# Kernel tuning notes

Hardware: AMD Instinct MI355X
Metric: run time of the kernel (lower is better)

Reference implementation:

```python
import jax, jax.numpy as jnp
import numpy as np
import math

N_FUNC = 32
LR_START, LR_DECAY = 1.0, 0.977
WEIGHT_DECAY, AMP_DECAY, MM_LR = 0.01, 0.01, 0.03
N_SAMP, BATCH, MOMENTUM = 32, 16, 0.85
N_FEAT, N_TARGET, MEM_SIZE = 1024, 512, 16384
DATA_SIZE = 100
SQRT_NF = math.sqrt(N_FUNC)


def setup_inputs() -> dict:
    key = jax.random.key(0)
    ks = jax.random.split(key, 16)
    p = jnp.linspace(0.01, 0.99, N_FUNC)[:, None]
    center_freq = jnp.log(p / (1.0 - p))  # logit of linspace, as in __init__
    return {
        "t": DATA_SIZE,
        "data_size": DATA_SIZE,
        "ts": jax.random.randint(ks[0], (N_SAMP,), 0, DATA_SIZE + 1),
        "x": jax.random.normal(ks[1], (N_FEAT,), jnp.float32),
        "z": jax.random.normal(ks[2], (N_TARGET,), jnp.float32),
        "memory": jax.random.normal(ks[3], (MEM_SIZE, N_TARGET), jnp.float32),
        "t_memory": jax.random.randint(ks[4], (MEM_SIZE,), 0, DATA_SIZE),
        "feat_memory": jax.random.normal(ks[5], (MEM_SIZE, N_FEAT), jnp.float32),
        "amp_re": 1.0 / SQRT_NF + 0.01 * jax.random.normal(ks[6], (N_FUNC, N_TARGET), jnp.float32),
        "amp_im": 0.01 * jax.random.normal(ks[7], (N_FUNC, N_TARGET), jnp.float32),
        "freq": 0.1 * jax.random.normal(ks[8], (N_FUNC, 1), jnp.float32),
        "center_freq": center_freq.astype(jnp.float32),
        "res_proj": 0.02 * jax.random.normal(ks[9], (N_FEAT + N_TARGET, N_TARGET), jnp.float32),
        "feat_mean": 0.1 * jax.random.normal(ks[10], (N_FEAT,), jnp.float32),
        "bias": 0.1 * jax.random.normal(ks[11], (N_TARGET,), jnp.float32),
        "amp_grad_re": 0.01 * jax.random.normal(ks[12], (N_FUNC, N_TARGET), jnp.float32),
        "amp_grad_im": 0.01 * jax.random.normal(ks[13], (N_FUNC, N_TARGET), jnp.float32),
        "freq_grad": 0.01 * jax.random.normal(ks[14], (N_FUNC, 1), jnp.float32),
        "res_proj_grad": 0.001 * jax.random.normal(ks[15], (N_FEAT + N_TARGET, N_TARGET), jnp.float32),
    }


def _get_freq(freq, center_freq):
    fr = center_freq + jnp.tanh(freq) * (64.0 / N_FUNC)
    return jax.nn.sigmoid(fr) * 0.5


def _evaluate(t, amp_re, amp_im, freq, bias, center_freq):
    # t: [B]; amp: [F, T]; freq/center_freq: [F, 1]
    fr = _get_freq(freq, center_freq)                      # [F, 1]
    ph = (2.0 * math.pi) * t[:, None, None] * fr           # [B, F, 1]
    # Re(exp(i*ph) * (amp_re + i*amp_im)) = cos*amp_re - sin*amp_im
    z = (jnp.cos(ph) * amp_re - jnp.sin(ph) * amp_im).sum(1) / SQRT_NF
    return z + bias                                        # [B, T]


def _get_resid(x, z, res_proj, feat_mean, bias):
    r = jnp.concatenate([x - feat_mean, z - bias], axis=-1) @ res_proj
    return r / (jnp.abs(r) + 1.0)


def reference(t, data_size, ts, x, z, memory, t_memory, feat_memory,
              amp_re, amp_im, freq, center_freq, res_proj, feat_mean, bias,
              amp_grad_re, amp_grad_im, freq_grad, res_proj_grad):
    # scatter new sample into the ring buffers
    memory = memory.at[data_size].set(z)
    feat_memory = feat_memory.at[data_size].set(x)
    t_memory = t_memory.at[data_size].set(t)
    ds_new = data_size + 1
    lr = LR_START * LR_DECAY ** ds_new  # lr after this call's decay
    # running means (torch uses the already-incremented data_size)
    bias = (bias * ds_new + z) / (ds_new + 1)
    feat_mean = (feat_mean * ds_new + x) / (ds_new + 1)

    for b in range(N_SAMP // BATCH):
        batch = ts[b * BATCH:(b + 1) * BATCH]
        t_b = t_memory[batch].astype(jnp.float32)
        z_b = memory[batch]
        x_b = feat_memory[batch]

        def loss_fn(a_re, a_im, fq, rp):
            z_ = _evaluate(t_b, a_re, a_im, fq, bias, center_freq)
            amp_abs = jnp.sqrt(a_re ** 2 + a_im ** 2)
            loss = jnp.sqrt(amp_abs).sum() * AMP_DECAY
            loss = loss + jnp.abs(z_b - z_).sum(-1).mean()
            resid = _get_resid(x_b, z_, rp, feat_mean, bias)
            z2 = jax.lax.stop_gradient(z_) + resid
            res_loss = jnp.abs(z_b - z2).sum(-1).mean()
            # torch uses self.res_proj (buffer) here -> no grad through this term
            res_loss = res_loss + jnp.abs(jax.lax.stop_gradient(rp)).sum() * WEIGHT_DECAY
            return loss + res_loss * MM_LR

        ag_re, ag_im, fg, rg = jax.grad(loss_fn, argnums=(0, 1, 2, 3))(amp_re, amp_im, freq, res_proj)
        # momentum decay then normalized-grad accumulate, then SGD step
        anorm = jnp.sqrt((ag_re ** 2).sum() + (ag_im ** 2).sum()) + 1.0  # complex vector norm
        amp_grad_re = amp_grad_re * MOMENTUM + ag_re / anorm
        amp_grad_im = amp_grad_im * MOMENTUM + ag_im / anorm
        amp_re = amp_re - amp_grad_re * lr
        amp_im = amp_im - amp_grad_im * lr
        fnorm = jnp.sqrt((fg ** 2).sum()) + 1.0
        freq_grad = freq_grad * MOMENTUM + fg / fnorm
        freq = freq - freq_grad * lr
        rnorm = jnp.sqrt((rg ** 2).sum()) + 1.0
        res_proj_grad = res_proj_grad * MOMENTUM + rg / rnorm
        res_proj = res_proj - res_proj_grad * lr

    return (memory, t_memory, feat_memory, amp_re, amp_im, freq, res_proj,
            bias, feat_mean, amp_grad_re, amp_grad_im, freq_grad, res_proj_grad)
```

## Files before the change

kernel.cpp:

```cpp
#include <hip/hip_runtime.h>
#include <math.h>

#define NT 512
#define NF 1024
#define NFUNC 32
#define BATCHSZ 16

typedef float v4f __attribute__((ext_vector_type(4)));
typedef int   v4i __attribute__((ext_vector_type(4)));

constexpr int O_MEM  = 0;
constexpr int O_TMEM = 8388608;
constexpr int O_FEAT = 8404992;
constexpr int O_ARE  = 25182208;
constexpr int O_AIM  = 25198592;
constexpr int O_FREQ = 25214976;
constexpr int O_RP   = 25215008;
constexpr int O_BIAS = 26001440;
constexpr int O_FM   = 26001952;
constexpr int O_AGR  = 26002976;
constexpr int O_AGI  = 26019360;
constexpr int O_FGR  = 26035744;
constexpr int O_RPG  = 26035776;

constexpr int W_LR    = 0;
constexpr int W_ANORM = 2;
constexpr int W_RNORM = 4;
constexpr int W_GFR   = 8;
constexpr int W_TB    = 72;
constexpr int W_C     = 96;
constexpr int W_S     = 608;
constexpr int W_CATZ  = 1120;
constexpr int W_CATX  = 9312;
constexpr int W_GR    = 25696;
constexpr int W_G     = 33888;
constexpr int W_AGRE  = 42080;
constexpr int W_AGIM  = 58464;
constexpr int W_RPART = 74848;

constexpr float MM_LR = 0.03f;
constexpr float AMP_DECAY = 0.01f;
constexpr float MOM = 0.85f;
constexpr float INV_SQRT_NF = 0.17677669529663687f;
constexpr float TWO_PI = 6.283185307179586f;

constexpr int NCOPY = 256;
constexpr long long U_TOTAL = 6295552LL;

constexpr int R_MEM_END  = 2097152;
constexpr int R_FEAT_END = 6291456;
constexpr int R_TM_END   = 6295552;

__device__ __forceinline__ float sgnf(float x) {
    return (x > 0.f) ? 1.f : ((x < 0.f) ? -1.f : 0.f);
}

__device__ __forceinline__ float wave_reduce(float v) {
#pragma unroll
    for (int o = 32; o > 0; o >>= 1) v += __shfl_down(v, o, 64);
    return v;
}

__device__ __forceinline__ void copy_role(int rb, int cbase, int ccnt,
    const int* __restrict__ tptr, const int* __restrict__ dsptr,
    const float* __restrict__ x, const float* __restrict__ z,
    const float* __restrict__ memory, const int* __restrict__ t_memory,
    const float* __restrict__ feat_memory, float* __restrict__ out)
{
    const int dsv  = *dsptr;
    const int nthr = NCOPY * 256;
    const int tg   = rb * 256 + (int)threadIdx.x;
    const int cend = cbase + ccnt;

    {
        const int a1 = cend < R_MEM_END ? cend : R_MEM_END;
        const v4f* __restrict__ src = (const v4f*)memory;
        const v4f* __restrict__ zz  = (const v4f*)z;
        v4f* __restrict__ dst = (v4f*)(out + O_MEM);
        int u = cbase + tg;
        for (; u + 3 * nthr < a1; u += 4 * nthr) {
            const int u1 = u + nthr, u2 = u + 2 * nthr, u3 = u + 3 * nthr;
            v4f v0 = __builtin_nontemporal_load((u  >> 7) == dsv ? zz + (u  & 127) : src + u );
            v4f v1 = __builtin_nontemporal_load((u1 >> 7) == dsv ? zz + (u1 & 127) : src + u1);
            v4f v2 = __builtin_nontemporal_load((u2 >> 7) == dsv ? zz + (u2 & 127) : src + u2);
            v4f v3 = __builtin_nontemporal_load((u3 >> 7) == dsv ? zz + (u3 & 127) : src + u3);
            __builtin_nontemporal_store(v0, dst + u );
            __builtin_nontemporal_store(v1, dst + u1);
            __builtin_nontemporal_store(v2, dst + u2);
            __builtin_nontemporal_store(v3, dst + u3);
        }
        for (; u < a1; u += nthr) {
            v4f v = __builtin_nontemporal_load((u >> 7) == dsv ? zz + (u & 127) : src + u);
            __builtin_nontemporal_store(v, dst + u);
        }
    }
    {
        const int a0 = cbase > R_MEM_END ? cbase : R_MEM_END;
        const int a1 = cend < R_FEAT_END ? cend : R_FEAT_END;
        const v4f* __restrict__ src = (const v4f*)feat_memory;
        const v4f* __restrict__ xx  = (const v4f*)x;
        v4f* __restrict__ dst = (v4f*)(out + O_FEAT);
        int u = a0 + tg;
        for (; u + 3 * nthr < a1; u += 4 * nthr) {
            const int u1 = u + nthr, u2 = u + 2 * nthr, u3 = u + 3 * nthr;
            const int f0 = u - R_MEM_END, f1 = u1 - R_MEM_END,
                      f2 = u2 - R_MEM_END, f3 = u3 - R_MEM_END;
            v4f v0 = __builtin_nontemporal_load((f0 >> 8) == dsv ? xx + (f0 & 255) : src + f0);
            v4f v1 = __builtin_nontemporal_load((f1 >> 8) == dsv ? xx + (f1 & 255) : src + f1);
            v4f v2 = __builtin_nontemporal_load((f2 >> 8) == dsv ? xx + (f2 & 255) : src + f2);
            v4f v3 = __builtin_nontemporal_load((f3 >> 8) == dsv ? xx + (f3 & 255) : src + f3);
            __builtin_nontemporal_store(v0, dst + f0);
            __builtin_nontemporal_store(v1, dst + f1);
            __builtin_nontemporal_store(v2, dst + f2);
            __builtin_nontemporal_store(v3, dst + f3);
        }
        for (; u < a1; u += nthr) {
            const int f = u - R_MEM_END;
            v4f v = __builtin_nontemporal_load((f >> 8) == dsv ? xx + (f & 255) : src + f);
            __builtin_nontemporal_store(v, dst + f);
        }
    }
    {
        const int a0 = cbase > R_FEAT_END ? cbase : R_FEAT_END;
        const int a1 = cend;
        if (a1 > a0) {
            const float ft = (float)(*tptr);
            const v4i* __restrict__ tm = (const v4i*)t_memory;
            v4f* __restrict__ dst = (v4f*)(out + O_TMEM);
            for (int u = a0 + tg; u < a1; u += nthr) {
                const int f = u - R_FEAT_END;
                const v4i iv = __builtin_nontemporal_load(tm + f);
                const int e = f * 4;
                v4f v;
                v.x = (e + 0 == dsv) ? ft : (float)iv.x;
                v.y = (e + 1 == dsv) ? ft : (float)iv.y;
                v.z = (e + 2 == dsv) ? ft : (float)iv.z;
                v.w = (e + 3 == dsv) ? ft : (float)iv.w;
                __builtin_nontemporal_store(v, dst + f);
            }
        }
    }
}

#define COPY_ARGS const int* __restrict__ tptr, const int* __restrict__ dsptr,            \
                  const float* __restrict__ x, const float* __restrict__ z,               \
                  const float* __restrict__ memory, const int* __restrict__ t_memory,     \
                  const float* __restrict__ feat_memory, int cbase, int ccnt
#define COPY_PASS tptr, dsptr, x, z, memory, t_memory, feat_memory

__global__ __launch_bounds__(256) void k_fwd_ab(int b, const int* __restrict__ ts,
    const float* __restrict__ cf,
    const float* __restrict__ are_src, const float* __restrict__ aim_src,
    const float* __restrict__ fq_src, const float* __restrict__ fm_in,
    const float* __restrict__ rp_src,
    float* __restrict__ out, float* __restrict__ ws, COPY_ARGS)
{
    int bb = blockIdx.x;
    const int tid = threadIdx.x;
    if (bb < NCOPY) { copy_role(bb, cbase, ccnt, COPY_PASS, out); return; }
    bb -= NCOPY;
    const int i = bb >> 4, s = bb & 15;
    __shared__ float c_l[32], s_l[32], cat[96];
    const int dsv = *dsptr;
    const int bi = ts[b * BATCHSZ + i];
    if (tid < 32) {
        float f  = fq_src[tid];
        float th = tanhf(f);
        float u  = cf[tid] + 2.f * th;
        float sg = 1.f / (1.f + expf(-u));
        float fr = 0.5f * sg;
        float tb = (bi == dsv) ? (float)(*tptr) : (float)t_memory[bi];
        float ph = TWO_PI * tb * fr;
        float cv = cosf(ph), sv = sinf(ph);
        c_l[tid] = cv; s_l[tid] = sv;
        if (s == 0) {
            ws[W_C + i*32 + tid] = cv; ws[W_S + i*32 + tid] = sv;
            if (tid == 0) ws[W_TB + i] = tb;
        }
    }
    if (bb == 0) {
        if (tid == 64) ws[W_ANORM + b] = 0.f;
        if (tid == 65) ws[W_RNORM + b] = 0.f;
        if (tid == 66 && b == 0) ws[W_LR] = (float)pow(0.977, (double)(dsv + 1));
        if (tid >= 96 && tid < 128) ws[W_GFR + b*32 + tid - 96] = 0.f;
    }
    __syncthreads();
    if (tid < 96) {
        int p = s * 96 + tid;
        float cv;
        if (p < NF) {
            const float nn = (float)(dsv + 1), dd = (float)(dsv + 2);
            float fmv = (fm_in[p] * nn + x[p]) / dd;
            float xv  = (bi == dsv) ? x[p] : feat_memory[bi*NF + p];
            cv = xv - fmv;
            ws[W_CATX + i*NF + p] = cv;
        } else {
            int q = p - NF;
            float acc = 0.f;
#pragma unroll
            for (int k = 0; k < 32; ++k)
                acc += c_l[k] * are_src[k*NT + q] - s_l[k] * aim_src[k*NT + q];
            cv = acc * INV_SQRT_NF;
            ws[W_CATZ + i*NT + q] = cv;
        }
        cat[tid] = cv;
    }
    __syncthreads();
    const int j = tid;
    const float* rpb = rp_src + (size_t)s * 96 * NT;
    float a0 = 0.f, a1 = 0.f, b0 = 0.f, b1 = 0.f;
#pragma unroll 8
    for (int p = 0; p < 96; p += 2) {
        float c0 = cat[p], c1 = cat[p + 1];
        a0 += c0 * rpb[p*NT + j];
        a1 += c0 * rpb[p*NT + j + 256];
        b0 += c1 * rpb[(p+1)*NT + j];
        b1 += c1 * rpb[(p+1)*NT + j + 256];
    }
    ws[W_RPART + s*8192 + i*NT + j]       = a0 + b0;
    ws[W_RPART + s*8192 + i*NT + j + 256] = a1 + b1;
}

__global__ __launch_bounds__(256) void k_eplg3(int b, const int* __restrict__ ts,
    const float* __restrict__ bias_in, const float* __restrict__ fm_in,
    const float* __restrict__ rp_src,
    float* __restrict__ out, float* __restrict__ ws, COPY_ARGS)
{
    int bb = blockIdx.x;
    const int tid = threadIdx.x;
    if (bb < NCOPY) { copy_role(bb, cbase, ccnt, COPY_PASS, out); return; }
    bb -= NCOPY;
    const int i = bb >> 6, jg = bb & 63;
    __shared__ float g_sh[NT], d_sh[NT];
    const int dsv = *dsptr;
    const int bi = ts[b * BATCHSZ + i];
    const float nn = (float)(dsv + 1), dd = (float)(dsv + 2);
#pragma unroll
    for (int ll = 0; ll < 2; ++ll) {
        int l = tid + ll * 256;
        float r = 0.f;
#pragma unroll
        for (int s = 0; s < 16; ++s) r += ws[W_RPART + s*8192 + i*NT + l];
        float bn = (bias_in[l] * nn + z[l]) / dd;
        float zj = ws[W_CATZ + i*NT + l] + bn;
        float zb = (bi == dsv) ? z[l] : memory[bi*NT + l];
        float s1 = sgnf(zj - zb);
        float ar = fabsf(r) + 1.f;
        float z2 = zj + r / ar;
        float g  = sgnf(z2 - zb) * (MM_LR / 16.f) / (ar * ar);
        g_sh[l] = g; d_sh[l] = s1 * (1.f / 16.f);
        if (jg == 0) {
            ws[W_GR + i*NT + l] = g;
            if (b == 0 && i == 0) out[O_BIAS + l] = bn;
        }
    }
    if (b == 0 && jg == 0 && i < 2) {
#pragma unroll
        for (int ll = 0; ll < 2; ++ll) {
            int p = i * 512 + tid + ll * 256;
            out[O_FM + p] = (fm_in[p] * nn + x[p]) / dd;
        }
    }
    __syncthreads();
    const int w = tid >> 6, lane = tid & 63;
#pragma unroll
    for (int jj = 0; jj < 2; ++jj) {
        int j = jg * 8 + w * 2 + jj;
        const float* rrow = rp_src + (size_t)(NF + j) * NT;
        float acc = 0.f;
#pragma unroll
        for (int l = lane; l < NT; l += 64) acc += g_sh[l] * rrow[l];
        acc = wave_reduce(acc);
        if (lane == 0) ws[W_G + i*NT + j] = d_sh[j] + acc;
    }
}

__global__ __launch_bounds__(256) void k_norms(int b,
    const float* __restrict__ are_src, const float* __restrict__ aim_src,
    float* __restrict__ out, float* __restrict__ ws, COPY_ARGS)
{
    __shared__ float red[4];
    int bb = blockIdx.x;
    const int tid = threadIdx.x;
    if (bb < NCOPY) { copy_role(bb, cbase, ccnt, COPY_PASS, out); return; }
    bb -= NCOPY;
    if (bb < 64) {
        int e = bb*256 + tid;
        int k = e >> 9;
        float gre = 0.f, gim = 0.f;
#pragma unroll
        for (int i2 = 0; i2 < 16; ++i2) {
            float G = ws[W_G + i2*NT + (e & 511)];
            gre += G * ws[W_C + i2*32 + k];
            gim += G * ws[W_S + i2*32 + k];
        }
        float re = are_src[e], im = aim_src[e];
        float aa = sqrtf(re*re + im*im);
        float dec = AMP_DECAY / (2.f * aa * sqrtf(aa));
        float agr =  gre * INV_SQRT_NF + re * dec;
        float agi = -gim * INV_SQRT_NF + im * dec;
        ws[W_AGRE + e] = agr;
        ws[W_AGIM + e] = agi;
        float v = wave_reduce(agr*agr + agi*agi);
        if ((tid & 63) == 0) red[tid >> 6] = v;
        __syncthreads();
        if (tid == 0) atomicAdd(&ws[W_ANORM + b], red[0]+red[1]+red[2]+red[3]);
    } else if (bb < 192) {
        int wid = tid >> 6, lane = tid & 63;
        int pair = (bb - 64)*4 + wid;
        int i = pair >> 5, k = pair & 31;
        float ck = ws[W_C + i*32 + k], sk = ws[W_S + i*32 + k];
        float acc = 0.f;
#pragma unroll
        for (int j = lane; j < NT; j += 64)
            acc += ws[W_G + i*NT + j] * (-sk * are_src[k*NT + j] - ck * aim_src[k*NT + j]);
        acc = wave_reduce(acc);
        if (lane == 0)
            atomicAdd(&ws[W_GFR + b*32 + k], acc * TWO_PI * ws[W_TB + i] * INV_SQRT_NF);
    } else {
        int e = (bb - 192)*256 + tid;
        int p = e >> 9, j = e & 511;
        float rg = 0.f;
#pragma unroll
        for (int i2 = 0; i2 < 16; ++i2) {
            float cat = (p < NF) ? ws[W_CATX + i2*NF + p]
                                 : ws[W_CATZ + i2*NT + (p - NF)];
            rg += cat * ws[W_GR + i2*NT + j];
        }
        float v = wave_reduce(rg * rg);
        if ((tid & 63) == 0) red[tid >> 6] = v;
        __syncthreads();
        if (tid == 0) atomicAdd(&ws[W_RNORM + b], red[0]+red[1]+red[2]+red[3]);
    }
}

__global__ __launch_bounds__(256) void k_upd(int b, const float* __restrict__ cf,
    const float* __restrict__ are_src, const float* __restrict__ aim_src,
    const float* __restrict__ agr_src, const float* __restrict__ agi_src,
    const float* __restrict__ fq_src,  const float* __restrict__ fgr_src,
    const float* __restrict__ rp_src,  const float* __restrict__ rpg_src,
    float* __restrict__ out, float* __restrict__ ws, COPY_ARGS)
{
    int bb = blockIdx.x;
    const int tid = threadIdx.x;
    if (bb < NCOPY) { copy_role(bb, cbase, ccnt, COPY_PASS, out); return; }
    bb -= NCOPY;
    const float lr = ws[W_LR];
    if (bb < 64) {
        int e = bb*256 + tid;
        float anorm = sqrtf(ws[W_ANORM + b]) + 1.f;
        float mr = agr_src[e]*MOM + ws[W_AGRE + e]/anorm;
        out[O_AGR + e] = mr; out[O_ARE + e] = are_src[e] - mr*lr;
        float mi = agi_src[e]*MOM + ws[W_AGIM + e]/anorm;
        out[O_AGI + e] = mi; out[O_AIM + e] = aim_src[e] - mi*lr;
    } else if (bb == 64) {
        if (tid < 64) {
            float fg = 0.f, th = 0.f;
            if (tid < 32) {
                float f = fq_src[tid];
                th = tanhf(f);
                float u  = cf[tid] + 2.f*th;
                float sg = 1.f / (1.f + expf(-u));
                fg = ws[W_GFR + b*32 + tid] * sg*(1.f-sg)*(1.f-th*th);
            }
            float t2 = fg*fg;
#pragma unroll
            for (int o = 32; o > 0; o >>= 1) t2 += __shfl_down(t2, o, 64);
            float tot = __shfl(t2, 0, 64);
            if (tid < 32) {
                float fnorm = sqrtf(tot) + 1.f;
                float m = fgr_src[tid]*MOM + fg/fnorm;
                out[O_FGR + tid] = m;
                out[O_FREQ + tid] = fq_src[tid] - m*lr;
            }
        }
    } else {
        int e = (bb - 65)*256 + tid;
        int p = e >> 9, j = e & 511;
        float rg = 0.f;
#pragma unroll
        for (int i2 = 0; i2 < 16; ++i2) {
            float cat = (p < NF) ? ws[W_CATX + i2*NF + p]
                                 : ws[W_CATZ + i2*NT + (p - NF)];
            rg += cat * ws[W_GR + i2*NT + j];
        }
        float rnorm = sqrtf(ws[W_RNORM + b]) + 1.f;
        float m = rpg_src[e]*MOM + rg/rnorm;
        out[O_RPG + e] = m; out[O_RP + e] = rp_src[e] - m*lr;
    }
}

extern "C" void kernel_launch(void* const* d_in, const int* in_sizes, int n_in,
                              void* d_out, int out_size, void* d_ws, size_t ws_size,
                              hipStream_t stream)
{
    const int*   t            = (const int*)d_in[0];
    const int*   dsp          = (const int*)d_in[1];
    const int*   ts           = (const int*)d_in[2];
    const float* x            = (const float*)d_in[3];
    const float* z            = (const float*)d_in[4];
    const float* memory       = (const float*)d_in[5];
    const int*   t_memory     = (const int*)d_in[6];
    const float* feat_memory  = (const float*)d_in[7];
    const float* amp_re       = (const float*)d_in[8];
    const float* amp_im       = (const float*)d_in[9];
    const float* freq         = (const float*)d_in[10];
    const float* cf           = (const float*)d_in[11];
    const float* res_proj     = (const float*)d_in[12];
    const float* feat_mean    = (const float*)d_in[13];
    const float* bias         = (const float*)d_in[14];
    const float* amp_grad_re  = (const float*)d_in[15];
    const float* amp_grad_im  = (const float*)d_in[16];
    const float* freq_grad    = (const float*)d_in[17];
    const float* res_proj_grad= (const float*)d_in[18];
    float* out = (float*)d_out;
    float* ws  = (float*)d_ws;

    const float* ARE[2] = { amp_re,        out + O_ARE };
    const float* AIM[2] = { amp_im,        out + O_AIM };
    const float* AGR[2] = { amp_grad_re,   out + O_AGR };
    const float* AGI[2] = { amp_grad_im,   out + O_AGI };
    const float* FQ [2] = { freq,          out + O_FREQ };
    const float* FGR[2] = { freq_grad,     out + O_FGR };
    const float* RP [2] = { res_proj,      out + O_RP };
    const float* RPG[2] = { res_proj_grad, out + O_RPG };

    const int per = 786944;
    int base = 0;
    auto nxt = [&](int& cb, int& cc) { cb = base; cc = per; base += cc; };
    int cb, cc;
    for (int b = 0; b < 2; ++b) {
        nxt(cb, cc);
        k_fwd_ab<<<256 + NCOPY, 256, 0, stream>>>(b, ts, cf, ARE[b], AIM[b], FQ[b],
            feat_mean, RP[b], out, ws, t, dsp, x, z, memory, t_memory, feat_memory, cb, cc);
        nxt(cb, cc);
        k_eplg3<<<1024 + NCOPY, 256, 0, stream>>>(b, ts, bias, feat_mean, RP[b], out, ws,
            t, dsp, x, z, memory, t_memory, feat_memory, cb, cc);
        nxt(cb, cc);
        k_norms<<<3264 + NCOPY, 256, 0, stream>>>(b, ARE[b], AIM[b], out, ws,
            t, dsp, x, z, memory, t_memory, feat_memory, cb, cc);
        nxt(cb, cc);
        k_upd<<<3137 + NCOPY, 256, 0, stream>>>(b, cf, ARE[b], AIM[b], AGR[b], AGI[b],
            FQ[b], FGR[b], RP[b], RPG[b], out, ws,
            t, dsp, x, z, memory, t_memory, feat_memory, cb, cc);
    }
}
```

Before: 333.1 us.

## Fuse multi-kernel training step into one cooperative persistent kernel with grid syncs

Replaces the sequence of per-stage kernel launches (two iterations, several stages each) with a single cooperative kernel of 512 blocks. Grid-wide syncs act as the stage boundaries, and the bulk memory copy is split into chunks placed between stages to overlap with compute. The aim is to remove launch overhead and inter-kernel gaps. In exchange it adds grid-barrier costs, halves the copy-loop unroll, and depends on cooperative launch support, falling back to the old path if that is missing.

```diff
diff --git a/kernel.cpp b/kernel.cpp
--- a/kernel.cpp
+++ b/kernel.cpp
@@ -1,5 +1,8 @@
 #include <hip/hip_runtime.h>
+#include <hip/hip_cooperative_groups.h>
 #include <math.h>
+
+namespace cg = cooperative_groups;
 
 #define NT 512
 #define NF 1024
@@ -44,12 +47,22 @@
 constexpr float INV_SQRT_NF = 0.17677669529663687f;
 constexpr float TWO_PI = 6.283185307179586f;
 
+constexpr int NB = 512;
+constexpr int CHUNK = 786944;
 constexpr int NCOPY = 256;
-constexpr long long U_TOTAL = 6295552LL;
 
 constexpr int R_MEM_END  = 2097152;
 constexpr int R_FEAT_END = 6291456;
-constexpr int R_TM_END   = 6295552;
+
+struct KParams {
+    const int *t, *dsp, *ts;
+    const float *x, *z, *memory;
+    const int *t_memory;
+    const float *feat_memory;
+    const float *amp_re, *amp_im, *freq, *cf, *res_proj, *feat_mean, *bias;
+    const float *amp_grad_re, *amp_grad_im, *freq_grad, *res_proj_grad;
+    float *out, *ws;
+};
 
 __device__ __forceinline__ float sgnf(float x) {
     return (x > 0.f) ? 1.f : ((x < 0.f) ? -1.f : 0.f);
@@ -61,33 +74,24 @@
     return v;
 }
 
-__device__ __forceinline__ void copy_role(int rb, int cbase, int ccnt,
-    const int* __restrict__ tptr, const int* __restrict__ dsptr,
+__device__ __forceinline__ void copy_span(int tg, int nthr, int cbase, int cend,
+    int dsv, int tt,
     const float* __restrict__ x, const float* __restrict__ z,
     const float* __restrict__ memory, const int* __restrict__ t_memory,
     const float* __restrict__ feat_memory, float* __restrict__ out)
 {
-    const int dsv  = *dsptr;
-    const int nthr = NCOPY * 256;
-    const int tg   = rb * 256 + (int)threadIdx.x;
-    const int cend = cbase + ccnt;
-
     {
         const int a1 = cend < R_MEM_END ? cend : R_MEM_END;
         const v4f* __restrict__ src = (const v4f*)memory;
         const v4f* __restrict__ zz  = (const v4f*)z;
         v4f* __restrict__ dst = (v4f*)(out + O_MEM);
         int u = cbase + tg;
-        for (; u + 3 * nthr < a1; u += 4 * nthr) {
-            const int u1 = u + nthr, u2 = u + 2 * nthr, u3 = u + 3 * nthr;
+        for (; u + nthr < a1; u += 2 * nthr) {
+            const int u1 = u + nthr;
             v4f v0 = __builtin_nontemporal_load((u  >> 7) == dsv ? zz + (u  & 127) : src + u );
             v4f v1 = __builtin_nontemporal_load((u1 >> 7) == dsv ? zz + (u1 & 127) : src + u1);
-            v4f v2 = __builtin_nontemporal_load((u2 >> 7) == dsv ? zz + (u2 & 127) : src + u2);
-            v4f v3 = __builtin_nontemporal_load((u3 >> 7) == dsv ? zz + (u3 & 127) : src + u3);
             __builtin_nontemporal_store(v0, dst + u );
             __builtin_nontemporal_store(v1, dst + u1);
-            __builtin_nontemporal_store(v2, dst + u2);
-            __builtin_nontemporal_store(v3, dst + u3);
         }
         for (; u < a1; u += nthr) {
             v4f v = __builtin_nontemporal_load((u >> 7) == dsv ? zz + (u & 127) : src + u);
@@ -101,18 +105,13 @@
         const v4f* __restrict__ xx  = (const v4f*)x;
         v4f* __restrict__ dst = (v4f*)(out + O_FEAT);
         int u = a0 + tg;
-        for (; u + 3 * nthr < a1; u += 4 * nthr) {
-            const int u1 = u + nthr, u2 = u + 2 * nthr, u3 = u + 3 * nthr;
-            const int f0 = u - R_MEM_END, f1 = u1 - R_MEM_END,
-                      f2 = u2 - R_MEM_END, f3 = u3 - R_MEM_END;
+        for (; u + nthr < a1; u += 2 * nthr) {
+            const int u1 = u + nthr;
+            const int f0 = u - R_MEM_END, f1 = u1 - R_MEM_END;
             v4f v0 = __builtin_nontemporal_load((f0 >> 8) == dsv ? xx + (f0 & 255) : src + f0);
             v4f v1 = __builtin_nontemporal_load((f1 >> 8) == dsv ? xx + (f1 & 255) : src + f1);
-            v4f v2 = __builtin_nontemporal_load((f2 >> 8) == dsv ? xx + (f2 & 255) : src + f2);
-            v4f v3 = __builtin_nontemporal_load((f3 >> 8) == dsv ? xx + (f3 & 255) : src + f3);
             __builtin_nontemporal_store(v0, dst + f0);
             __builtin_nontemporal_store(v1, dst + f1);
-            __builtin_nontemporal_store(v2, dst + f2);
-            __builtin_nontemporal_store(v3, dst + f3);
         }
         for (; u < a1; u += nthr) {
             const int f = u - R_MEM_END;
@@ -124,7 +123,7 @@
         const int a0 = cbase > R_FEAT_END ? cbase : R_FEAT_END;
         const int a1 = cend;
         if (a1 > a0) {
-            const float ft = (float)(*tptr);
+            const float ft = (float)tt;
             const v4i* __restrict__ tm = (const v4i*)t_memory;
             v4f* __restrict__ dst = (v4f*)(out + O_TMEM);
             for (int u = a0 + tg; u < a1; u += nthr) {
@@ -140,6 +139,276 @@
             }
         }
     }
+}
+
+__global__ __launch_bounds__(256, 2) void k_fused(KParams p)
+{
+    cg::grid_group grid = cg::this_grid();
+    const int bidx = (int)blockIdx.x;
+    const int tid  = (int)threadIdx.x;
+
+    __shared__ float c_l[32], s_l[32], cat[96];
+    __shared__ float g_sh[NT], d_sh[NT];
+    __shared__ float red[4];
+
+    float* __restrict__ out = p.out;
+    float* __restrict__ ws  = p.ws;
+    const int dsv = *p.dsp;
+    const int tt  = *p.t;
+    const float nn = (float)(dsv + 1), dd = (float)(dsv + 2);
+    const int tg   = bidx * 256 + tid;
+    const int nthr = NB * 256;
+
+    for (int b = 0; b < 2; ++b) {
+        const float* __restrict__ are_src = b ? out + O_ARE : p.amp_re;
+        const float* __restrict__ aim_src = b ? out + O_AIM : p.amp_im;
+        const float* __restrict__ fq_src  = b ? out + O_FREQ: p.freq;
+        const float* __restrict__ rp_src  = b ? out + O_RP  : p.res_proj;
+        const float* __restrict__ agr_src = b ? out + O_AGR : p.amp_grad_re;
+        const float* __restrict__ agi_src = b ? out + O_AGI : p.amp_grad_im;
+        const float* __restrict__ fgr_src = b ? out + O_FGR : p.freq_grad;
+        const float* __restrict__ rpg_src = b ? out + O_RPG : p.res_proj_grad;
+
+        if (bidx < 256) {
+            const int i = bidx >> 4, s = bidx & 15;
+            const int bi = p.ts[b * BATCHSZ + i];
+            if (tid < 32) {
+                float f  = fq_src[tid];
+                float th = tanhf(f);
+                float u  = p.cf[tid] + 2.f * th;
+                float sg = 1.f / (1.f + expf(-u));
+                float fr = 0.5f * sg;
+                float tb = (bi == dsv) ? (float)tt : (float)p.t_memory[bi];
+                float ph = TWO_PI * tb * fr;
+                float cv = cosf(ph), sv = sinf(ph);
+                c_l[tid] = cv; s_l[tid] = sv;
+                if (s == 0) {
+                    ws[W_C + i*32 + tid] = cv; ws[W_S + i*32 + tid] = sv;
+                    if (tid == 0) ws[W_TB + i] = tb;
+                }
+            }
+            if (bidx == 0) {
+                if (tid == 64) ws[W_ANORM + b] = 0.f;
+                if (tid == 65) ws[W_RNORM + b] = 0.f;
+                if (tid == 66 && b == 0) ws[W_LR] = (float)pow(0.977, (double)(dsv + 1));
+                if (tid >= 96 && tid < 128) ws[W_GFR + b*32 + tid - 96] = 0.f;
+            }
+            __syncthreads();
+            if (tid < 96) {
+                int pe = s * 96 + tid;
+                float cv;
+                if (pe < NF) {
+                    float fmv = (p.feat_mean[pe] * nn + p.x[pe]) / dd;
+                    float xv  = (bi == dsv) ? p.x[pe] : p.feat_memory[bi*NF + pe];
+                    cv = xv - fmv;
+                    ws[W_CATX + i*NF + pe] = cv;
+                } else {
+                    int q = pe - NF;
+                    float acc = 0.f;
+#pragma unroll
+                    for (int k = 0; k < 32; ++k)
+                        acc += c_l[k] * are_src[k*NT + q] - s_l[k] * aim_src[k*NT + q];
+                    cv = acc * INV_SQRT_NF;
+                    ws[W_CATZ + i*NT + q] = cv;
+                }
+                cat[tid] = cv;
+            }
+            __syncthreads();
+            const int j = tid;
+            const float* rpb = rp_src + (size_t)s * 96 * NT;
+            float a0 = 0.f, a1 = 0.f, b0 = 0.f, b1 = 0.f;
+#pragma unroll 8
+            for (int pp = 0; pp < 96; pp += 2) {
+                float c0 = cat[pp], c1 = cat[pp + 1];
+                a0 += c0 * rpb[pp*NT + j];
+                a1 += c0 * rpb[pp*NT + j + 256];
+                b0 += c1 * rpb[(pp+1)*NT + j];
+                b1 += c1 * rpb[(pp+1)*NT + j + 256];
+            }
+            ws[W_RPART + s*8192 + i*NT + j]       = a0 + b0;
+            ws[W_RPART + s*8192 + i*NT + j + 256] = a1 + b1;
+        }
+        {
+            int cb = (b*4 + 0) * CHUNK;
+            copy_span(tg, nthr, cb, cb + CHUNK, dsv, tt, p.x, p.z, p.memory, p.t_memory, p.feat_memory, out);
+        }
+        __threadfence();
+        grid.sync();
+        __threadfence();
+
+        for (int vb = bidx; vb < 1024; vb += NB) {
+            const int i = vb >> 6, jg = vb & 63;
+            const int bi = p.ts[b * BATCHSZ + i];
+#pragma unroll
+            for (int ll = 0; ll < 2; ++ll) {
+                int l = tid + ll * 256;
+                float r = 0.f;
+#pragma unroll
+                for (int s = 0; s < 16; ++s) r += ws[W_RPART + s*8192 + i*NT + l];
+                float bn = (p.bias[l] * nn + p.z[l]) / dd;
+                float zj = ws[W_CATZ + i*NT + l] + bn;
+                float zb = (bi == dsv) ? p.z[l] : p.memory[bi*NT + l];
+                float s1 = sgnf(zj - zb);
+                float ar = fabsf(r) + 1.f;
+                float z2 = zj + r / ar;
+                float g  = sgnf(z2 - zb) * (MM_LR / 16.f) / (ar * ar);
+                g_sh[l] = g; d_sh[l] = s1 * (1.f / 16.f);
+                if (jg == 0) {
+                    ws[W_GR + i*NT + l] = g;
+                    if (b == 0 && i == 0) out[O_BIAS + l] = bn;
+                }
+            }
+            if (b == 0 && jg == 0 && i < 2) {
+#pragma unroll
+                for (int ll = 0; ll < 2; ++ll) {
+                    int pe = i * 512 + tid + ll * 256;
+                    out[O_FM + pe] = (p.feat_mean[pe] * nn + p.x[pe]) / dd;
+                }
+            }
+            __syncthreads();
+            const int w = tid >> 6, lane = tid & 63;
+#pragma unroll
+            for (int jj = 0; jj < 2; ++jj) {
+                int j = jg * 8 + w * 2 + jj;
+                const float* rrow = rp_src + (size_t)(NF + j) * NT;
+                float acc = 0.f;
+#pragma unroll
+                for (int l = lane; l < NT; l += 64) acc += g_sh[l] * rrow[l];
+                acc = wave_reduce(acc);
+                if (lane == 0) ws[W_G + i*NT + j] = d_sh[j] + acc;
+            }
+            __syncthreads();
+        }
+        {
+            int cb = (b*4 + 1) * CHUNK;
+            copy_span(tg, nthr, cb, cb + CHUNK, dsv, tt, p.x, p.z, p.memory, p.t_memory, p.feat_memory, out);
+        }
+        __threadfence();
+        grid.sync();
+        __threadfence();
+
+        for (int it = bidx; it < 3264; it += NB) {
+            if (it < 64) {
+                int e = it*256 + tid;
+                int k = e >> 9;
+                float gre = 0.f, gim = 0.f;
+#pragma unroll
+                for (int i2 = 0; i2 < 16; ++i2) {
+                    float G = ws[W_G + i2*NT + (e & 511)];
+                    gre += G * ws[W_C + i2*32 + k];
+                    gim += G * ws[W_S + i2*32 + k];
+                }
+                float re = are_src[e], im = aim_src[e];
+                float aa = sqrtf(re*re + im*im);
+                float dec = AMP_DECAY / (2.f * aa * sqrtf(aa));
+                float agr =  gre * INV_SQRT_NF + re * dec;
+                float agi = -gim * INV_SQRT_NF + im * dec;
+                ws[W_AGRE + e] = agr;
+                ws[W_AGIM + e] = agi;
+                float v = wave_reduce(agr*agr + agi*agi);
+                if ((tid & 63) == 0) red[tid >> 6] = v;
+                __syncthreads();
+                if (tid == 0) atomicAdd(&ws[W_ANORM + b], red[0]+red[1]+red[2]+red[3]);
+            } else if (it < 192) {
+                int wid = tid >> 6, lane = tid & 63;
+                int pair = (it - 64)*4 + wid;
+                int i = pair >> 5, k = pair & 31;
+                float ck = ws[W_C + i*32 + k], sk = ws[W_S + i*32 + k];
+                float acc = 0.f;
+#pragma unroll
+                for (int j = lane; j < NT; j += 64)
+                    acc += ws[W_G + i*NT + j] * (-sk * are_src[k*NT + j] - ck * aim_src[k*NT + j]);
+                acc = wave_reduce(acc);
+                if (lane == 0)
+                    atomicAdd(&ws[W_GFR + b*32 + k], acc * TWO_PI * ws[W_TB + i] * INV_SQRT_NF);
+            } else {
+                int e = (it - 192)*256 + tid;
+                int pr = e >> 9, j = e & 511;
+                float rg = 0.f;
+#pragma unroll
+                for (int i2 = 0; i2 < 16; ++i2) {
+                    float cv = (pr < NF) ? ws[W_CATX + i2*NF + pr]
+                                         : ws[W_CATZ + i2*NT + (pr - NF)];
+                    rg += cv * ws[W_GR + i2*NT + j];
+                }
+                float v = wave_reduce(rg * rg);
+                if ((tid & 63) == 0) red[tid >> 6] = v;
+                __syncthreads();
+                if (tid == 0) atomicAdd(&ws[W_RNORM + b], red[0]+red[1]+red[2]+red[3]);
+            }
+            __syncthreads();
+        }
+        {
+            int cb = (b*4 + 2) * CHUNK;
+            copy_span(tg, nthr, cb, cb + CHUNK, dsv, tt, p.x, p.z, p.memory, p.t_memory, p.feat_memory, out);
+        }
+        __threadfence();
+        grid.sync();
+        __threadfence();
+
+        const float lr = ws[W_LR];
+        for (int it = bidx; it < 3137; it += NB) {
+            if (it < 64) {
+                int e = it*256 + tid;
+                float anorm = sqrtf(ws[W_ANORM + b]) + 1.f;
+                float mr = agr_src[e]*MOM + ws[W_AGRE + e]/anorm;
+                out[O_AGR + e] = mr; out[O_ARE + e] = are_src[e] - mr*lr;
+                float mi = agi_src[e]*MOM + ws[W_AGIM + e]/anorm;
+                out[O_AGI + e] = mi; out[O_AIM + e] = aim_src[e] - mi*lr;
+            } else if (it == 64) {
+                if (tid < 64) {
+                    float fg = 0.f, th = 0.f;
+                    if (tid < 32) {
+                        float f = fq_src[tid];
+                        th = tanhf(f);
+                        float u  = p.cf[tid] + 2.f*th;
+                        float sg = 1.f / (1.f + expf(-u));
+                        fg = ws[W_GFR + b*32 + tid] * sg*(1.f-sg)*(1.f-th*th);
+                    }
+                    float t2 = fg*fg;
+#pragma unroll
+                    for (int o = 32; o > 0; o >>= 1) t2 += __shfl_down(t2, o, 64);
+                    float tot = __shfl(t2, 0, 64);
+                    if (tid < 32) {
+                        float fnorm = sqrtf(tot) + 1.f;
+                        float m = fgr_src[tid]*MOM + fg/fnorm;
+                        out[O_FGR + tid] = m;
+                        out[O_FREQ + tid] = fq_src[tid] - m*lr;
+                    }
+                }
+            } else {
+                int e = (it - 65)*256 + tid;
+                int pr = e >> 9, j = e & 511;
+                float rg = 0.f;
+#pragma unroll
+                for (int i2 = 0; i2 < 16; ++i2) {
+                    float cv = (pr < NF) ? ws[W_CATX + i2*NF + pr]
+                                         : ws[W_CATZ + i2*NT + (pr - NF)];
+                    rg += cv * ws[W_GR + i2*NT + j];
+                }
+                float rnorm = sqrtf(ws[W_RNORM + b]) + 1.f;
+                float m = rpg_src[e]*MOM + rg/rnorm;
+                out[O_RPG + e] = m; out[O_RP + e] = rp_src[e] - m*lr;
+            }
+        }
+        {
+            int cb = (b*4 + 3) * CHUNK;
+            copy_span(tg, nthr, cb, cb + CHUNK, dsv, tt, p.x, p.z, p.memory, p.t_memory, p.feat_memory, out);
+        }
+        if (b == 0) { __threadfence(); grid.sync(); __threadfence(); }
+    }
+}
+
+__device__ __forceinline__ void copy_role(int rb, int cbase, int ccnt,
+    const int* __restrict__ tptr, const int* __restrict__ dsptr,
+    const float* __restrict__ x, const float* __restrict__ z,
+    const float* __restrict__ memory, const int* __restrict__ t_memory,
+    const float* __restrict__ feat_memory, float* __restrict__ out)
+{
+    const int dsv = *dsptr;
+    const int tt  = *tptr;
+    copy_span(rb * 256 + (int)threadIdx.x, NCOPY * 256, cbase, cbase + ccnt,
+              dsv, tt, x, z, memory, t_memory, feat_memory, out);
 }
 
 #define COPY_ARGS const int* __restrict__ tptr, const int* __restrict__ dsptr,            \
@@ -416,6 +685,34 @@
     float* out = (float*)d_out;
     float* ws  = (float*)d_ws;
 
+    static int coop_ok = -1;
+    if (coop_ok < 0) {
+        int dev = 0;
+        hipGetDevice(&dev);
+        hipDeviceProp_t prop;
+        int ok = (hipGetDeviceProperties(&prop, dev) == hipSuccess);
+        int maxb = 0;
+        if (ok) ok = (hipOccupancyMaxActiveBlocksPerMultiprocessor(&maxb, k_fused, 256, 0) == hipSuccess);
+        coop_ok = (ok && prop.cooperativeLaunch &&
+                   (long long)maxb * prop.multiProcessorCount >= NB) ? 1 : 0;
+    }
+
+    if (coop_ok == 1) {
+        KParams p;
+        p.t = t; p.dsp = dsp; p.ts = ts; p.x = x; p.z = z; p.memory = memory;
+        p.t_memory = t_memory; p.feat_memory = feat_memory;
+        p.amp_re = amp_re; p.amp_im = amp_im; p.freq = freq; p.cf = cf;
+        p.res_proj = res_proj; p.feat_mean = feat_mean; p.bias = bias;
+        p.amp_grad_re = amp_grad_re; p.amp_grad_im = amp_grad_im;
+        p.freq_grad = freq_grad; p.res_proj_grad = res_proj_grad;
+        p.out = out; p.ws = ws;
+        void* args[] = { (void*)&p };
+        hipError_t e = hipLaunchCooperativeKernel(reinterpret_cast<void*>(k_fused),
+                                                  dim3(NB), dim3(256), args, 0, stream);
+        if (e == hipSuccess) return;
+        coop_ok = 0;
+    }
+
     const float* ARE[2] = { amp_re,        out + O_ARE };
     const float* AIM[2] = { amp_im,        out + O_AIM };
     const float* AGR[2] = { amp_grad_re,   out + O_AGR };
```

After: 329.3 us. No clear change (-1.1%).
